# Performance work log

Measured on AMD Instinct MI355X. Metric: run time of the kernel, lower is better.

Reference implementation:

```python
import jax, jax.numpy as jnp
import numpy as np

B, S, D, H, DH, FF = 4, 4096, 1024, 16, 64, 2048
EPS = 1e-6


def setup_inputs() -> dict:
    key = jax.random.key(0)
    ks = jax.random.split(key, 8)
    s = 0.02
    return {
        "x": jax.random.normal(ks[0], (B, S, D), jnp.float32),
        "scale": jnp.ones((D,), jnp.float32),
        "qw": jax.random.normal(ks[1], (DH * H, D), jnp.float32) * s,
        "qb": jnp.zeros((DH * H,), jnp.float32),
        "kw": jax.random.normal(ks[2], (DH * H, D), jnp.float32) * s,
        "kb": jnp.zeros((DH * H,), jnp.float32),
        "vw": jax.random.normal(ks[3], (DH * H, D), jnp.float32) * s,
        "vb": jnp.zeros((DH * H,), jnp.float32),
        "ow": jax.random.normal(ks[4], (D, DH * H), jnp.float32) * s,
        "ob": jnp.zeros((D,), jnp.float32),
        "f1w": jax.random.normal(ks[5], (FF, D), jnp.float32) * s,
        "f1b": jnp.zeros((FF,), jnp.float32),
        "f2w": jax.random.normal(ks[6], (D, FF), jnp.float32) * s,
        "f2b": jnp.zeros((D,), jnp.float32),
    }


def reference(x, scale, qw, qb, kw, kb, vw, vb, ow, ob, f1w, f1b, f2w, f2b):
    def rms(h):
        return h / jnp.sqrt(jnp.mean(h * h, axis=-1, keepdims=True) + EPS) * scale

    # --- attention (faithful to the module's unusual permutes) ---
    xn = rms(x)
    q = (xn @ qw.T + qb).reshape(B, S, DH, H).transpose(0, 3, 2, 1)  # [B,H,DH,S]
    k = (xn @ kw.T + kb).reshape(B, S, DH, H).transpose(0, 3, 1, 2)  # [B,H,S,DH]
    v = (xn @ vw.T + vb).reshape(B, S, DH, H).transpose(0, 3, 2, 1)  # [B,H,DH,S]
    # scores contract over the SEQUENCE axis -> [B,H,DH,DH]
    att = jax.nn.softmax(jnp.einsum('bhds,bhse->bhde', q, k) / jnp.sqrt(jnp.float32(DH)), axis=-1)
    a = jnp.einsum('bhde,bhes->bhds', att, v)  # [B,H,DH,S]
    # torch: permute(0,2,1,3).reshape(B,-1,DH*H); row-major split of (DH,H,S) -> (S, DH*H)
    a = a.transpose(0, 2, 1, 3).reshape(B, S, DH * H)
    x = a @ ow.T + ob + x

    # --- FFN with the repo's 'SwiGLU' = x*sigmoid(x) + x ---
    xn = rms(x)
    h = xn @ f1w.T + f1b
    h = h * jax.nn.sigmoid(h) + h
    x = h @ f2w.T + f2b + x
    return x
```

## Files before the change

### kernel.cpp

```cpp
#include <hip/hip_runtime.h>
#include <math.h>

typedef unsigned short u16;
typedef __attribute__((ext_vector_type(4))) unsigned short us4;
typedef __attribute__((ext_vector_type(8))) unsigned short us8;
typedef __attribute__((ext_vector_type(4))) float f4;
typedef __attribute__((ext_vector_type(8))) short bf16x8;
typedef __attribute__((ext_vector_type(4))) float f32x4;

#define S_LEN   4096
#define D_MODEL 1024
#define N_HEAD  16
#define D_HEAD  64
#define FF_DIM  2048
#define TOKENS  16384

__device__ __forceinline__ float bf2f(u16 u) {
  union { float f; unsigned u; } x; x.u = ((unsigned)u) << 16; return x.f;
}
__device__ __forceinline__ u16 f2bf(float f) {
  union { float f; unsigned u; } x; x.f = f;
  return (u16)((x.u + 0x7FFFu + ((x.u >> 16) & 1u)) >> 16);
}

__device__ __forceinline__ void gll16(const void* g, void* l) {
  __builtin_amdgcn_global_load_lds(
      (const __attribute__((address_space(1))) void*)g,
      (__attribute__((address_space(3))) void*)l, 16, 0, 0);
}

#define BARF() do { __builtin_amdgcn_s_barrier(); asm volatile("" ::: "memory"); } while (0)

__global__ void __launch_bounds__(256)
cvt6_k(const float* __restrict__ qw, const float* __restrict__ kw,
       const float* __restrict__ vw, const float* __restrict__ ow,
       const float* __restrict__ f1w, const float* __restrict__ f2w,
       u16* __restrict__ wq, u16* __restrict__ wk, u16* __restrict__ wv,
       u16* __restrict__ wo, u16* __restrict__ w1, u16* __restrict__ w2)
{
  const int id = blockIdx.x;
  const float* src; u16* dst; int base;
  if      (id < 1024) { src = qw;  dst = wq; base = 0; }
  else if (id < 2048) { src = kw;  dst = wk; base = 1024; }
  else if (id < 3072) { src = vw;  dst = wv; base = 2048; }
  else if (id < 4096) { src = ow;  dst = wo; base = 3072; }
  else if (id < 6144) { src = f1w; dst = w1; base = 4096; }
  else                { src = f2w; dst = w2; base = 6144; }
  const size_t i = ((size_t)(id - base) * 256 + threadIdx.x) * 4;
  const f4 v = *(const f4*)(src + i);
  us4 o;
  o[0] = f2bf(v[0]); o[1] = f2bf(v[1]); o[2] = f2bf(v[2]); o[3] = f2bf(v[3]);
  *(us4*)(dst + i) = o;
}

__global__ void __launch_bounds__(256)
rmsnorm_k(const float* __restrict__ in, const float* __restrict__ scale,
          u16* __restrict__ out)
{
  const int row = blockIdx.x;
  const int tid = threadIdx.x;
  const f4 v = *(const f4*)(in + (size_t)row * D_MODEL + tid * 4);
  float ss = v[0]*v[0] + v[1]*v[1] + v[2]*v[2] + v[3]*v[3];
#pragma unroll
  for (int off = 32; off > 0; off >>= 1) ss += __shfl_down(ss, off, 64);
  __shared__ float red[4];
  const int wid = tid >> 6, lane = tid & 63;
  if (lane == 0) red[wid] = ss;
  __syncthreads();
  const float tot = red[0] + red[1] + red[2] + red[3];
  const float r = rsqrtf(tot * (1.0f / 1024.0f) + 1e-6f);
  const f4 sc = *(const f4*)(scale + tid * 4);
  us4 o;
  o[0] = f2bf(v[0] * r * sc[0]);
  o[1] = f2bf(v[1] * r * sc[1]);
  o[2] = f2bf(v[2] * r * sc[2]);
  o[3] = f2bf(v[3] * r * sc[3]);
  *(us4*)(out + (size_t)row * D_MODEL + tid * 4) = o;
}

template<int EPI>
__global__ __launch_bounds__(512, 2)
void g8k(const u16* __restrict__ Ag, const u16* __restrict__ Wg,
         const float* __restrict__ bq, const float* __restrict__ bk,
         const float* __restrict__ bv, const float* __restrict__ res,
         void* __restrict__ C0, void* __restrict__ C1, void* __restrict__ C2,
         int N, int K)
{
  __shared__ __align__(16) u16 lds[65536];
  const int tid = threadIdx.x;
  const int w = tid >> 6, l = tid & 63;
  const int fr = l & 15, fq = l >> 4;
  const int wm = w >> 2, wn = w & 3;
  const int m0 = blockIdx.x << 8, n0 = blockIdx.y << 8;
  const int srow = w * 8 + (l >> 3);
  const int scol = ((l & 7) ^ (l >> 3)) << 3;
  const int NT = K >> 6;

  auto STAGE = [&](int isA, int hf, int bfs, int nt) {
    const u16* G = isA ? Ag : Wg;
    const int rb = (isA ? m0 : n0) + hf * 128 + srow;
    const int ks = (nt < NT ? nt << 6 : 0) + scol;
    u16* lb = lds + (isA ? 0 : 32768) + bfs * 16384 + hf * 8192 + w * 512;
    gll16(G + (size_t)rb * K + ks, lb);
    gll16(G + (size_t)(rb + 64) * K + ks, lb + 4096);
  };

  f32x4 acc[8][4] = {};
  bf16x8 b_frag[4][2];

  auto LDB_ALL = [&](int bf) {
#pragma unroll
    for (int ni = 0; ni < 4; ++ni)
#pragma unroll
      for (int kk = 0; kk < 2; ++kk)
        b_frag[ni][kk] = *(const bf16x8*)(lds + 32768 + bf * 16384 + (ni >> 1) * 8192
                                          + ((ni & 1) * 64 + wn * 16 + fr) * 64
                                          + ((kk * 32 + fq * 8) ^ ((fr & 7) << 3)));
  };

  auto CHUNK = [&](int bf, int mh, int mi) {
    const u16* base = lds + bf * 16384 + mh * 8192 + (mi * 32 + wm * 16 + fr) * 64;
    const bf16x8 a0 = *(const bf16x8*)(base + ((fq * 8) ^ ((fr & 7) << 3)));
    const bf16x8 a1 = *(const bf16x8*)(base + ((32 + fq * 8) ^ ((fr & 7) << 3)));
    __builtin_amdgcn_s_setprio(1);
#pragma unroll
    for (int ni = 0; ni < 4; ++ni) {
      acc[mh * 4 + mi][ni] =
          __builtin_amdgcn_mfma_f32_16x16x32_bf16(a0, b_frag[ni][0], acc[mh * 4 + mi][ni], 0, 0, 0);
      acc[mh * 4 + mi][ni] =
          __builtin_amdgcn_mfma_f32_16x16x32_bf16(a1, b_frag[ni][1], acc[mh * 4 + mi][ni], 0, 0, 0);
    }
    __builtin_amdgcn_s_setprio(0);
  };

  STAGE(0, 0, 0, 0);
  STAGE(0, 1, 0, 0);
  STAGE(1, 0, 0, 0);
  STAGE(1, 1, 0, 0);
  asm volatile("s_waitcnt vmcnt(2)" ::: "memory");
  BARF();

#pragma unroll 2
  for (int t = 0; t < NT; ++t) {
    const int bf = t & 1;
    LDB_ALL(bf);
    STAGE(0, 0, bf ^ 1, t + 1);
    STAGE(0, 1, bf ^ 1, t + 1);
    CHUNK(bf, 0, 0); CHUNK(bf, 0, 1); CHUNK(bf, 0, 2); CHUNK(bf, 0, 3);
    asm volatile("s_waitcnt vmcnt(4)" ::: "memory");
    BARF();
    STAGE(1, 0, bf ^ 1, t + 1);
    STAGE(1, 1, bf ^ 1, t + 1);
    CHUNK(bf, 1, 0); CHUNK(bf, 1, 1); CHUNK(bf, 1, 2); CHUNK(bf, 1, 3);
    asm volatile("s_waitcnt vmcnt(2)" ::: "memory");
    BARF();
  }
  asm volatile("s_waitcnt vmcnt(0)" ::: "memory");
  __builtin_amdgcn_s_barrier();
  asm volatile("" ::: "memory");

  if constexpr (EPI == 2) {
    float* C = (float*)C0;
#pragma unroll
    for (int mi = 0; mi < 8; ++mi)
#pragma unroll
      for (int ni = 0; ni < 4; ++ni) {
        const int c = n0 + ni * 64 + wn * 16 + fr;
        const int r0 = m0 + mi * 32 + wm * 16 + fq * 4;
        const float bb = bq[c];
#pragma unroll
        for (int j = 0; j < 4; ++j)
          C[(size_t)(r0 + j) * N + c] = acc[mi][ni][j] + bb + res[(size_t)(r0 + j) * N + c];
      }
  } else if constexpr (EPI == 3) {
    u16* C = (u16*)C0;
#pragma unroll
    for (int mi = 0; mi < 8; ++mi)
#pragma unroll
      for (int ni = 0; ni < 4; ++ni) {
        const int c = n0 + ni * 64 + wn * 16 + fr;
        const int r0 = m0 + mi * 32 + wm * 16 + fq * 4;
        const float bb = bq[c];
#pragma unroll
        for (int j = 0; j < 4; ++j) {
          const float v = acc[mi][ni][j] + bb;
          const float sig = 1.0f / (1.0f + expf(-v));
          C[(size_t)(r0 + j) * N + c] = f2bf(v * sig + v);
        }
      }
  } else {
    const int z = blockIdx.y >> 2;
    const float* bias = z == 0 ? bq : (z == 1 ? bk : bv);
    const int n0l = n0 & 1023;
    const int bb = m0 >> 12, s0l = m0 & (S_LEN - 1);
#pragma unroll
    for (int mi = 0; mi < 8; ++mi)
#pragma unroll
      for (int ni = 0; ni < 4; ++ni) {
        const int c = ni * 64 + wn * 16 + fr;
        const int r0 = mi * 32 + wm * 16 + fq * 4;
        const float bv_ = bias[n0l + c];
        us4 pk;
#pragma unroll
        for (int j = 0; j < 4; ++j) pk[j] = f2bf(acc[mi][ni][j] + bv_);
        const int byte = ((c << 9) + (r0 << 1)) ^ ((c & 7) << 4);
        *(us4*)((char*)lds + byte) = pk;
      }
    __syncthreads();
    if (z < 2) {
      u16* Cout = z == 0 ? (u16*)C0 : (u16*)C1;
      const int c = tid & 255, half = tid >> 8;
      const int o = n0l + c, d = o >> 4, h = o & 15;
      const int xr = (c & 7) << 4;
      u16* dst = Cout + ((size_t)((bb << 10) + (h << 6) + d)) * S_LEN + s0l + half * 128;
#pragma unroll
      for (int u = 0; u < 16; ++u) {
        const int byte = ((c << 9) + (half << 8) + (u << 4)) ^ xr;
        const us8 v = *(const us8*)((char*)lds + byte);
        *(us8*)(dst + u * 8) = v;
      }
    } else {
      u16* Cv = (u16*)C2;
      const int d0 = n0l >> 4;
#pragma unroll
      for (int q2 = 0; q2 < 8; ++q2) {
        const int idx = q2 * 512 + tid;
        const int h = idx >> 8, r = idx & 255;
        const int xr = (h & 7) << 4;
        us8 lo, hi;
#pragma unroll
        for (int dl = 0; dl < 8; ++dl) {
          lo[dl] = *(const u16*)((char*)lds + ((((h + dl * 16) << 9) + (r << 1)) ^ xr));
          hi[dl] = *(const u16*)((char*)lds + ((((h + (dl + 8) * 16) << 9) + (r << 1)) ^ xr));
        }
        u16* dst = Cv + ((size_t)(bb * 16 + h) * S_LEN + s0l + r) * 64 + d0;
        *(us8*)dst = lo;
        *(us8*)(dst + 8) = hi;
      }
    }
  }
}

__global__ void __launch_bounds__(256)
att_sm_k(const u16* __restrict__ qt, const u16* __restrict__ kt,
         u16* __restrict__ P)
{
  __shared__ float red[4][64][64];
  const int bh = blockIdx.x;
  const int tid = threadIdx.x, w = tid >> 6, l = tid & 63;
  const int fr = l & 15, fq = l >> 4;
  const u16* Qb = qt + (size_t)bh * D_HEAD * S_LEN;
  const u16* Kb = kt + (size_t)bh * D_HEAD * S_LEN;
  f32x4 acc[4][4] = {};
  const int sb = w * 1024 + fq * 8;
  for (int ks = 0; ks < 32; ++ks) {
    const int s0 = sb + ks * 32;
    bf16x8 a[4], b[4];
#pragma unroll
    for (int m = 0; m < 4; ++m)
      a[m] = *(const bf16x8*)(Qb + (size_t)(m*16 + fr) * S_LEN + s0);
#pragma unroll
    for (int n = 0; n < 4; ++n)
      b[n] = *(const bf16x8*)(Kb + (size_t)(n*16 + fr) * S_LEN + s0);
#pragma unroll
    for (int m = 0; m < 4; ++m)
#pragma unroll
      for (int n = 0; n < 4; ++n)
        acc[m][n] = __builtin_amdgcn_mfma_f32_16x16x32_bf16(a[m], b[n], acc[m][n], 0, 0, 0);
  }
#pragma unroll
  for (int m = 0; m < 4; ++m)
#pragma unroll
    for (int n = 0; n < 4; ++n)
      *(f32x4*)&red[w][n*16 + fr][m*16 + fq*4] = acc[m][n];
  __syncthreads();

  const int d = tid >> 2, sub = tid & 3;
  float p[16];
  float mx = -1e30f;
#pragma unroll
  for (int i = 0; i < 16; ++i) {
    const int e = sub * 16 + i;
    float v = red[0][e][d] + red[1][e][d] + red[2][e][d] + red[3][e][d];
    v *= 0.125f;
    p[i] = v; mx = fmaxf(mx, v);
  }
  mx = fmaxf(mx, __shfl_xor(mx, 1, 64));
  mx = fmaxf(mx, __shfl_xor(mx, 2, 64));
  float sm = 0.0f;
#pragma unroll
  for (int i = 0; i < 16; ++i) { p[i] = expf(p[i] - mx); sm += p[i]; }
  sm += __shfl_xor(sm, 1, 64);
  sm += __shfl_xor(sm, 2, 64);
  const float inv = 1.0f / sm;
  us8 o0, o1;
#pragma unroll
  for (int i = 0; i < 8; ++i) { o0[i] = f2bf(p[i] * inv); o1[i] = f2bf(p[i+8] * inv); }
  u16* dst = P + (size_t)bh * 4096 + d * 64 + sub * 16;
  *(us8*)dst = o0;
  *(us8*)(dst + 8) = o1;
}

__global__ void __launch_bounds__(256)
pv2_k(const u16* __restrict__ P, const u16* __restrict__ v2,
      u16* __restrict__ ar)
{
  const int bh = blockIdx.x, sc = blockIdx.y;
  const int b = bh >> 4, h = bh & 15;
  const int tid = threadIdx.x, w = tid >> 6, l = tid & 63;
  const int fr = l & 15, fq = l >> 4;
  const u16* Pb = P + (size_t)bh * 4096;
  const u16* Vb = v2 + (size_t)bh * D_HEAD * S_LEN;

  bf16x8 a[4][2];
#pragma unroll
  for (int m = 0; m < 4; ++m)
#pragma unroll
    for (int ks = 0; ks < 2; ++ks)
      a[m][ks] = *(const bf16x8*)(Pb + (m*16 + fr) * 64 + ks*32 + fq*8);

  const int sw = sc * 512 + w * 128;
  f32x4 acc[8][4] = {};
#pragma unroll
  for (int n = 0; n < 8; ++n) {
    const u16* vp = Vb + (size_t)(sw + n*16 + fr) * 64 + fq*8;
    const bf16x8 b0 = *(const bf16x8*)(vp);
    const bf16x8 b1 = *(const bf16x8*)(vp + 32);
#pragma unroll
    for (int m = 0; m < 4; ++m)
      acc[n][m] = __builtin_amdgcn_mfma_f32_16x16x32_bf16(a[m][0], b0, acc[n][m], 0, 0, 0);
#pragma unroll
    for (int m = 0; m < 4; ++m)
      acc[n][m] = __builtin_amdgcn_mfma_f32_16x16x32_bf16(a[m][1], b1, acc[n][m], 0, 0, 0);
  }

  const int shi = sc >> 1;
  const int col0 = (sc & 1) * 512 + w * 128;
#pragma unroll
  for (int m = 0; m < 4; ++m)
#pragma unroll
    for (int j = 0; j < 4; ++j) {
      const int d = m*16 + fq*4 + j;
      const size_t base = ((size_t)b * 4096 + (d << 6) + (h << 2) + shi) * 1024 + col0;
#pragma unroll
      for (int n = 0; n < 8; ++n)
        ar[base + n*16 + fr] = f2bf(acc[n][m][j]);
    }
}

extern "C" void kernel_launch(void* const* d_in, const int* in_sizes, int n_in,
                              void* d_out, int out_size, void* d_ws, size_t ws_size,
                              hipStream_t stream)
{
  const float* x     = (const float*)d_in[0];
  const float* scale = (const float*)d_in[1];
  const float* qw = (const float*)d_in[2];
  const float* qb = (const float*)d_in[3];
  const float* kw = (const float*)d_in[4];
  const float* kb = (const float*)d_in[5];
  const float* vw = (const float*)d_in[6];
  const float* vb = (const float*)d_in[7];
  const float* ow = (const float*)d_in[8];
  const float* ob = (const float*)d_in[9];
  const float* f1w = (const float*)d_in[10];
  const float* f1b = (const float*)d_in[11];
  const float* f2w = (const float*)d_in[12];
  const float* f2b = (const float*)d_in[13];
  float* out = (float*)d_out;

  const size_t TOKD = (size_t)TOKENS * D_MODEL;
  const size_t WSZ1 = (size_t)D_MODEL * D_MODEL;
  const size_t WSZ2 = (size_t)FF_DIM * D_MODEL;
  u16* xn = (u16*)d_ws;
  u16* qt = xn + TOKD;
  u16* kt = qt + TOKD;
  u16* v2 = kt + TOKD;
  u16* wq = v2 + TOKD;
  u16* wk = wq + WSZ1;
  u16* wv = wk + WSZ1;
  u16* wo = wv + WSZ1;
  u16* w1 = wo + WSZ1;
  u16* w2 = w1 + WSZ2;
  u16* Patt = w2 + WSZ2;
  u16* hbuf = kt;
  u16* ar = qt;

  dim3 blk(256);
  dim3 blk8(512);

  cvt6_k<<<8192, blk, 0, stream>>>(qw, kw, vw, ow, f1w, f2w, wq, wk, wv, wo, w1, w2);
  rmsnorm_k<<<TOKENS, blk, 0, stream>>>(x, scale, xn);
  g8k<0><<<dim3(TOKENS / 256, 12), blk8, 0, stream>>>(
      xn, wq, qb, kb, vb, nullptr, qt, kt, v2, 3072, D_MODEL);
  att_sm_k<<<64, blk, 0, stream>>>(qt, kt, Patt);
  pv2_k<<<dim3(64, 8), blk, 0, stream>>>(Patt, v2, ar);
  g8k<2><<<dim3(TOKENS / 256, D_MODEL / 256), blk8, 0, stream>>>(
      ar, wo, ob, nullptr, nullptr, x, out, nullptr, nullptr, D_MODEL, D_MODEL);
  rmsnorm_k<<<TOKENS, blk, 0, stream>>>(out, scale, xn);
  g8k<3><<<dim3(TOKENS / 256, FF_DIM / 256), blk8, 0, stream>>>(
      xn, w1, f1b, nullptr, nullptr, nullptr, hbuf, nullptr, nullptr, FF_DIM, D_MODEL);
  g8k<2><<<dim3(TOKENS / 256, D_MODEL / 256), blk8, 0, stream>>>(
      hbuf, w2, f2b, nullptr, nullptr, out, out, nullptr, nullptr, D_MODEL, FF_DIM);
}
```

Measured before the change: 442.1 us.

## Shrink GEMM tile to 256x128 with K=32 triple-buffered pipeline

Reworks the bf16 MFMA GEMM from a 256x256 tile with K-step 64 and double buffering to a 256x128 tile with K-step 32 and a three-stage LDS ring. LDS use drops and launch bounds rise to allow more resident blocks, with grids doubled in N to match. The point is more occupancy and latency hiding through deeper prefetch. In exchange, each block reuses less data per tile, global traffic for A goes up, and there are more barriers per unit of K.

```diff
diff --git a/kernel.cpp b/kernel.cpp
--- a/kernel.cpp
+++ b/kernel.cpp
@@ -79,94 +79,78 @@
 }
 
 template<int EPI>
-__global__ __launch_bounds__(512, 2)
+__global__ __launch_bounds__(512, 4)
 void g8k(const u16* __restrict__ Ag, const u16* __restrict__ Wg,
          const float* __restrict__ bq, const float* __restrict__ bk,
          const float* __restrict__ bv, const float* __restrict__ res,
          void* __restrict__ C0, void* __restrict__ C1, void* __restrict__ C2,
          int N, int K)
 {
-  __shared__ __align__(16) u16 lds[65536];
+  __shared__ __align__(16) u16 lds[36864];
   const int tid = threadIdx.x;
   const int w = tid >> 6, l = tid & 63;
   const int fr = l & 15, fq = l >> 4;
-  const int wm = w >> 2, wn = w & 3;
-  const int m0 = blockIdx.x << 8, n0 = blockIdx.y << 8;
-  const int srow = w * 8 + (l >> 3);
-  const int scol = ((l & 7) ^ (l >> 3)) << 3;
-  const int NT = K >> 6;
-
-  auto STAGE = [&](int isA, int hf, int bfs, int nt) {
-    const u16* G = isA ? Ag : Wg;
-    const int rb = (isA ? m0 : n0) + hf * 128 + srow;
-    const int ks = (nt < NT ? nt << 6 : 0) + scol;
-    u16* lb = lds + (isA ? 0 : 32768) + bfs * 16384 + hf * 8192 + w * 512;
-    gll16(G + (size_t)rb * K + ks, lb);
-    gll16(G + (size_t)(rb + 64) * K + ks, lb + 4096);
+  const int wm = w >> 1, wn = w & 1;
+  const int m0 = blockIdx.x << 8, n0 = blockIdx.y << 7;
+  const int srow = w * 16 + (l >> 2);
+  const int scol = (((l & 3) ^ ((l >> 3) & 3)) << 3);
+  const int NT = K >> 5;
+
+  auto STAGE_A = [&](int bfs, int h, int nt) {
+    const int ks = (nt < NT ? nt << 5 : 0) + scol;
+    gll16(Ag + (size_t)(m0 + h * 128 + srow) * K + ks,
+          lds + bfs * 12288 + h * 4096 + w * 512);
   };
-
-  f32x4 acc[8][4] = {};
-  bf16x8 b_frag[4][2];
-
-  auto LDB_ALL = [&](int bf) {
+  auto STAGE_B = [&](int bfs, int nt) {
+    const int ks = (nt < NT ? nt << 5 : 0) + scol;
+    gll16(Wg + (size_t)(n0 + srow) * K + ks,
+          lds + bfs * 12288 + 8192 + w * 512);
+  };
+
+  f32x4 acc[4][4] = {};
+  bf16x8 afr[4], bfr[4];
+  const int rsw = (fq ^ ((fr >> 1) & 3)) << 3;
+  const int abase = (wm * 64 + fr) * 32 + rsw;
+  const int bbase = 8192 + (wn * 64 + fr) * 32 + rsw;
+
+  STAGE_A(0, 0, 0); STAGE_A(0, 1, 0); STAGE_B(0, 0);
+  STAGE_A(1, 0, 1); STAGE_A(1, 1, 1); STAGE_B(1, 1);
+  asm volatile("s_waitcnt vmcnt(3)" ::: "memory");
+  BARF();
+
+#pragma unroll 3
+  for (int t = 0; t < NT; ++t) {
+    const int buf = t % 3, buf2 = (t + 2) % 3;
+    const int bo = buf * 12288;
+#pragma unroll
+    for (int mi = 0; mi < 4; ++mi)
+      afr[mi] = *(const bf16x8*)(lds + bo + abase + mi * 512);
 #pragma unroll
     for (int ni = 0; ni < 4; ++ni)
-#pragma unroll
-      for (int kk = 0; kk < 2; ++kk)
-        b_frag[ni][kk] = *(const bf16x8*)(lds + 32768 + bf * 16384 + (ni >> 1) * 8192
-                                          + ((ni & 1) * 64 + wn * 16 + fr) * 64
-                                          + ((kk * 32 + fq * 8) ^ ((fr & 7) << 3)));
-  };
-
-  auto CHUNK = [&](int bf, int mh, int mi) {
-    const u16* base = lds + bf * 16384 + mh * 8192 + (mi * 32 + wm * 16 + fr) * 64;
-    const bf16x8 a0 = *(const bf16x8*)(base + ((fq * 8) ^ ((fr & 7) << 3)));
-    const bf16x8 a1 = *(const bf16x8*)(base + ((32 + fq * 8) ^ ((fr & 7) << 3)));
+      bfr[ni] = *(const bf16x8*)(lds + bo + bbase + ni * 512);
+    STAGE_A(buf2, 0, t + 2); STAGE_A(buf2, 1, t + 2); STAGE_B(buf2, t + 2);
     __builtin_amdgcn_s_setprio(1);
 #pragma unroll
-    for (int ni = 0; ni < 4; ++ni) {
-      acc[mh * 4 + mi][ni] =
-          __builtin_amdgcn_mfma_f32_16x16x32_bf16(a0, b_frag[ni][0], acc[mh * 4 + mi][ni], 0, 0, 0);
-      acc[mh * 4 + mi][ni] =
-          __builtin_amdgcn_mfma_f32_16x16x32_bf16(a1, b_frag[ni][1], acc[mh * 4 + mi][ni], 0, 0, 0);
-    }
+    for (int mi = 0; mi < 4; ++mi)
+#pragma unroll
+      for (int ni = 0; ni < 4; ++ni)
+        acc[mi][ni] = __builtin_amdgcn_mfma_f32_16x16x32_bf16(afr[mi], bfr[ni],
+                                                              acc[mi][ni], 0, 0, 0);
     __builtin_amdgcn_s_setprio(0);
-  };
-
-  STAGE(0, 0, 0, 0);
-  STAGE(0, 1, 0, 0);
-  STAGE(1, 0, 0, 0);
-  STAGE(1, 1, 0, 0);
-  asm volatile("s_waitcnt vmcnt(2)" ::: "memory");
-  BARF();
-
-#pragma unroll 2
-  for (int t = 0; t < NT; ++t) {
-    const int bf = t & 1;
-    LDB_ALL(bf);
-    STAGE(0, 0, bf ^ 1, t + 1);
-    STAGE(0, 1, bf ^ 1, t + 1);
-    CHUNK(bf, 0, 0); CHUNK(bf, 0, 1); CHUNK(bf, 0, 2); CHUNK(bf, 0, 3);
-    asm volatile("s_waitcnt vmcnt(4)" ::: "memory");
+    asm volatile("s_waitcnt vmcnt(3)" ::: "memory");
     BARF();
-    STAGE(1, 0, bf ^ 1, t + 1);
-    STAGE(1, 1, bf ^ 1, t + 1);
-    CHUNK(bf, 1, 0); CHUNK(bf, 1, 1); CHUNK(bf, 1, 2); CHUNK(bf, 1, 3);
-    asm volatile("s_waitcnt vmcnt(2)" ::: "memory");
-    BARF();
   }
   asm volatile("s_waitcnt vmcnt(0)" ::: "memory");
-  __builtin_amdgcn_s_barrier();
-  asm volatile("" ::: "memory");
+  __syncthreads();
 
   if constexpr (EPI == 2) {
     float* C = (float*)C0;
 #pragma unroll
-    for (int mi = 0; mi < 8; ++mi)
+    for (int mi = 0; mi < 4; ++mi)
 #pragma unroll
       for (int ni = 0; ni < 4; ++ni) {
-        const int c = n0 + ni * 64 + wn * 16 + fr;
-        const int r0 = m0 + mi * 32 + wm * 16 + fq * 4;
+        const int c = n0 + wn * 64 + ni * 16 + fr;
+        const int r0 = m0 + wm * 64 + mi * 16 + fq * 4;
         const float bb = bq[c];
 #pragma unroll
         for (int j = 0; j < 4; ++j)
@@ -175,11 +159,11 @@
   } else if constexpr (EPI == 3) {
     u16* C = (u16*)C0;
 #pragma unroll
-    for (int mi = 0; mi < 8; ++mi)
+    for (int mi = 0; mi < 4; ++mi)
 #pragma unroll
       for (int ni = 0; ni < 4; ++ni) {
-        const int c = n0 + ni * 64 + wn * 16 + fr;
-        const int r0 = m0 + mi * 32 + wm * 16 + fq * 4;
+        const int c = n0 + wn * 64 + ni * 16 + fr;
+        const int r0 = m0 + wm * 64 + mi * 16 + fq * 4;
         const float bb = bq[c];
 #pragma unroll
         for (int j = 0; j < 4; ++j) {
@@ -189,16 +173,16 @@
         }
       }
   } else {
-    const int z = blockIdx.y >> 2;
+    const int z = blockIdx.y >> 3;
     const float* bias = z == 0 ? bq : (z == 1 ? bk : bv);
     const int n0l = n0 & 1023;
     const int bb = m0 >> 12, s0l = m0 & (S_LEN - 1);
 #pragma unroll
-    for (int mi = 0; mi < 8; ++mi)
+    for (int mi = 0; mi < 4; ++mi)
 #pragma unroll
       for (int ni = 0; ni < 4; ++ni) {
-        const int c = ni * 64 + wn * 16 + fr;
-        const int r0 = mi * 32 + wm * 16 + fq * 4;
+        const int c = wn * 64 + ni * 16 + fr;
+        const int r0 = wm * 64 + mi * 16 + fq * 4;
         const float bv_ = bias[n0l + c];
         us4 pk;
 #pragma unroll
@@ -209,13 +193,13 @@
     __syncthreads();
     if (z < 2) {
       u16* Cout = z == 0 ? (u16*)C0 : (u16*)C1;
-      const int c = tid & 255, half = tid >> 8;
+      const int c = tid & 127, sb = tid >> 7;
       const int o = n0l + c, d = o >> 4, h = o & 15;
       const int xr = (c & 7) << 4;
-      u16* dst = Cout + ((size_t)((bb << 10) + (h << 6) + d)) * S_LEN + s0l + half * 128;
-#pragma unroll
-      for (int u = 0; u < 16; ++u) {
-        const int byte = ((c << 9) + (half << 8) + (u << 4)) ^ xr;
+      u16* dst = Cout + ((size_t)((bb << 10) + (h << 6) + d)) * S_LEN + s0l + sb * 64;
+#pragma unroll
+      for (int u = 0; u < 8; ++u) {
+        const int byte = ((c << 9) + (sb << 7) + (u << 4)) ^ xr;
         const us8 v = *(const us8*)((char*)lds + byte);
         *(us8*)(dst + u * 8) = v;
       }
@@ -223,19 +207,16 @@
       u16* Cv = (u16*)C2;
       const int d0 = n0l >> 4;
 #pragma unroll
-      for (int q2 = 0; q2 < 8; ++q2) {
-        const int idx = q2 * 512 + tid;
-        const int h = idx >> 8, r = idx & 255;
+      for (int q = 0; q < 8; ++q) {
+        const int idx = q * 512 + tid;
+        const int h = idx >> 8, s = idx & 255;
         const int xr = (h & 7) << 4;
-        us8 lo, hi;
-#pragma unroll
-        for (int dl = 0; dl < 8; ++dl) {
-          lo[dl] = *(const u16*)((char*)lds + ((((h + dl * 16) << 9) + (r << 1)) ^ xr));
-          hi[dl] = *(const u16*)((char*)lds + ((((h + (dl + 8) * 16) << 9) + (r << 1)) ^ xr));
-        }
-        u16* dst = Cv + ((size_t)(bb * 16 + h) * S_LEN + s0l + r) * 64 + d0;
-        *(us8*)dst = lo;
-        *(us8*)(dst + 8) = hi;
+        us8 o;
+#pragma unroll
+        for (int k = 0; k < 8; ++k)
+          o[k] = *(const u16*)((char*)lds + ((((h + k * 16) << 9) + (s << 1)) ^ xr));
+        u16* dst = Cv + ((size_t)(bb * 16 + h) * S_LEN + s0l + s) * 64 + d0;
+        *(us8*)dst = o;
       }
     }
   }
@@ -390,15 +371,15 @@
 
   cvt6_k<<<8192, blk, 0, stream>>>(qw, kw, vw, ow, f1w, f2w, wq, wk, wv, wo, w1, w2);
   rmsnorm_k<<<TOKENS, blk, 0, stream>>>(x, scale, xn);
-  g8k<0><<<dim3(TOKENS / 256, 12), blk8, 0, stream>>>(
+  g8k<0><<<dim3(TOKENS / 256, 24), blk8, 0, stream>>>(
       xn, wq, qb, kb, vb, nullptr, qt, kt, v2, 3072, D_MODEL);
   att_sm_k<<<64, blk, 0, stream>>>(qt, kt, Patt);
   pv2_k<<<dim3(64, 8), blk, 0, stream>>>(Patt, v2, ar);
-  g8k<2><<<dim3(TOKENS / 256, D_MODEL / 256), blk8, 0, stream>>>(
+  g8k<2><<<dim3(TOKENS / 256, D_MODEL / 128), blk8, 0, stream>>>(
       ar, wo, ob, nullptr, nullptr, x, out, nullptr, nullptr, D_MODEL, D_MODEL);
   rmsnorm_k<<<TOKENS, blk, 0, stream>>>(out, scale, xn);
-  g8k<3><<<dim3(TOKENS / 256, FF_DIM / 256), blk8, 0, stream>>>(
+  g8k<3><<<dim3(TOKENS / 256, FF_DIM / 128), blk8, 0, stream>>>(
       xn, w1, f1b, nullptr, nullptr, nullptr, hbuf, nullptr, nullptr, FF_DIM, D_MODEL);
-  g8k<2><<<dim3(TOKENS / 256, D_MODEL / 256), blk8, 0, stream>>>(
+  g8k<2><<<dim3(TOKENS / 256, D_MODEL / 128), blk8, 0, stream>>>(
       hbuf, w2, f2b, nullptr, nullptr, out, out, nullptr, nullptr, D_MODEL, FF_DIM);
 }
```

New measurement: 495.3 us. 1.12x slower.

## Store GEMM tiles in LDS in MFMA fragment order and prefetch second B tile

Applied to the files above, without the earlier changes.

Replaces the XOR-swizzled row-major LDS tile layout with a fragment-ordered layout. Each global-to-LDS load now brings in a 16-row by 64-byte block, so every lane's MFMA operand is a contiguous 16-byte read at lane*8 with no address swizzle math. The prologue also issues the B tile for the second k-step early. That B tile is reloaded again in the first loop iteration, so the extra loads are redundant traffic. Global loads become narrower per row (64B segments instead of 128B), which may reduce coalescing efficiency.

```diff
diff --git a/kernel.cpp b/kernel.cpp
--- a/kernel.cpp
+++ b/kernel.cpp
@@ -92,17 +92,21 @@
   const int fr = l & 15, fq = l >> 4;
   const int wm = w >> 2, wn = w & 3;
   const int m0 = blockIdx.x << 8, n0 = blockIdx.y << 8;
-  const int srow = w * 8 + (l >> 3);
-  const int scol = ((l & 7) ^ (l >> 3)) << 3;
   const int NT = K >> 6;
 
   auto STAGE = [&](int isA, int hf, int bfs, int nt) {
     const u16* G = isA ? Ag : Wg;
-    const int rb = (isA ? m0 : n0) + hf * 128 + srow;
-    const int ks = (nt < NT ? nt << 6 : 0) + scol;
-    u16* lb = lds + (isA ? 0 : 32768) + bfs * 16384 + hf * 8192 + w * 512;
-    gll16(G + (size_t)rb * K + ks, lb);
-    gll16(G + (size_t)(rb + 64) * K + ks, lb + 4096);
+    const int rbase = (isA ? m0 : n0);
+    const int kb = (nt < NT ? nt << 6 : 0);
+    u16* region = lds + (isA ? 0 : 32768) + bfs * 16384;
+#pragma unroll
+    for (int j = 0; j < 2; ++j) {
+      const int f = hf * 16 + j * 8 + w;
+      const int rg = f >> 1, kk = f & 1;
+      const int row = rbase + rg * 16 + fr;
+      const int col = kb + kk * 32 + fq * 8;
+      gll16(G + (size_t)row * K + col, region + f * 512);
+    }
   };
 
   f32x4 acc[8][4] = {};
@@ -112,16 +116,18 @@
 #pragma unroll
     for (int ni = 0; ni < 4; ++ni)
 #pragma unroll
-      for (int kk = 0; kk < 2; ++kk)
-        b_frag[ni][kk] = *(const bf16x8*)(lds + 32768 + bf * 16384 + (ni >> 1) * 8192
-                                          + ((ni & 1) * 64 + wn * 16 + fr) * 64
-                                          + ((kk * 32 + fq * 8) ^ ((fr & 7) << 3)));
+      for (int kk = 0; kk < 2; ++kk) {
+        const int rg = (ni >> 1) * 8 + (ni & 1) * 4 + wn;
+        b_frag[ni][kk] = *(const bf16x8*)(lds + 32768 + bf * 16384
+                                          + rg * 1024 + kk * 512 + l * 8);
+      }
   };
 
   auto CHUNK = [&](int bf, int mh, int mi) {
-    const u16* base = lds + bf * 16384 + mh * 8192 + (mi * 32 + wm * 16 + fr) * 64;
-    const bf16x8 a0 = *(const bf16x8*)(base + ((fq * 8) ^ ((fr & 7) << 3)));
-    const bf16x8 a1 = *(const bf16x8*)(base + ((32 + fq * 8) ^ ((fr & 7) << 3)));
+    const int rg = mh * 8 + mi * 2 + wm;
+    const u16* base = lds + bf * 16384 + rg * 1024 + l * 8;
+    const bf16x8 a0 = *(const bf16x8*)(base);
+    const bf16x8 a1 = *(const bf16x8*)(base + 512);
     __builtin_amdgcn_s_setprio(1);
 #pragma unroll
     for (int ni = 0; ni < 4; ++ni) {
@@ -137,6 +143,8 @@
   STAGE(0, 1, 0, 0);
   STAGE(1, 0, 0, 0);
   STAGE(1, 1, 0, 0);
+  STAGE(1, 0, 1, 1);
+  STAGE(1, 1, 1, 1);
   asm volatile("s_waitcnt vmcnt(2)" ::: "memory");
   BARF();
 
```

Result: slower. 507.5 us (+14.8%).
